# Kernel tuning notes

Measured on AMD Instinct MI355X. Metric: run time of the kernel, lower is better.

## Reference

```python
import jax, jax.numpy as jnp
import numpy as np

B = 2
D = 256
NH = 8
DH = D // NH
LV = 4
NP_ = 4
NL = 6
DFF = 1024
SHAPES = [(112, 112), (56, 56), (28, 28), (14, 14)]
S = sum(h * w for h, w in SHAPES)


def setup_inputs() -> dict:
    key = jax.random.key(0)
    ks = iter(jax.random.split(key, 64))
    d = {}
    for i, (h, w) in enumerate(SHAPES):
        d[f"src{i}"] = jax.random.normal(next(ks), (B, D, h, w), jnp.float32)
        d[f"pos{i}"] = jax.random.normal(next(ks), (B, D, h, w), jnp.float32)

    def W(*shape, scale=0.02):
        return jax.random.normal(next(ks), shape, jnp.float32) * scale

    d["level_embed"] = W(LV, D, scale=1.0)
    d["off_w"] = W(NL, D, NH * LV * NP_ * 2)
    d["off_b"] = W(NL, NH * LV * NP_ * 2, scale=0.5)
    d["aw_w"] = W(NL, D, NH * LV * NP_)
    d["aw_b"] = jnp.zeros((NL, NH * LV * NP_), jnp.float32)
    d["val_w"] = W(NL, D, D)
    d["val_b"] = jnp.zeros((NL, D), jnp.float32)
    d["out_w"] = W(NL, D, D)
    d["out_b"] = jnp.zeros((NL, D), jnp.float32)
    d["ln1_s"] = jnp.ones((NL, D), jnp.float32)
    d["ln1_b"] = jnp.zeros((NL, D), jnp.float32)
    d["ff1_w"] = W(NL, D, DFF)
    d["ff1_b"] = jnp.zeros((NL, DFF), jnp.float32)
    d["ff2_w"] = W(NL, DFF, D)
    d["ff2_b"] = jnp.zeros((NL, D), jnp.float32)
    d["ln2_s"] = jnp.ones((NL, D), jnp.float32)
    d["ln2_b"] = jnp.zeros((NL, D), jnp.float32)
    return d


def _ln(x, s, b):
    m = jnp.mean(x, -1, keepdims=True)
    v = jnp.mean((x - m) ** 2, -1, keepdims=True)
    return (x - m) / jnp.sqrt(v + 1e-5) * s + b


def _bilinear(v, loc, Hl, Wl):
    # v: [N, DH, Hl, Wl]; loc: [N, Q, P, 2] in [0,1] (grid_sample align_corners=False, zero padding)
    N, Dh = v.shape[0], v.shape[1]
    Q, P = loc.shape[1], loc.shape[2]
    x = loc[..., 0] * Wl - 0.5
    y = loc[..., 1] * Hl - 0.5
    x0f = jnp.floor(x)
    y0f = jnp.floor(y)
    lx = x - x0f
    ly = y - y0f
    x0 = x0f.astype(jnp.int32)
    y0 = y0f.astype(jnp.int32)
    vf = v.reshape(N, Dh, Hl * Wl)

    def g(xi, yi):
        valid = (xi >= 0) & (xi < Wl) & (yi >= 0) & (yi < Hl)
        idx = (jnp.clip(yi, 0, Hl - 1) * Wl + jnp.clip(xi, 0, Wl - 1)).reshape(N, Q * P)
        out = jnp.take_along_axis(vf, idx[:, None, :], axis=2).reshape(N, Dh, Q, P)
        return out * valid[:, None].astype(v.dtype)

    w00 = ((1 - lx) * (1 - ly))[:, None]
    w10 = (lx * (1 - ly))[:, None]
    w01 = ((1 - lx) * ly)[:, None]
    w11 = (lx * ly)[:, None]
    return g(x0, y0) * w00 + g(x0 + 1, y0) * w10 + g(x0, y0 + 1) * w01 + g(x0 + 1, y0 + 1) * w11


def _ms_deform_attn(value, loc, attn):
    # value [B,S,NH,DH], loc [B,S,NH,LV,P,2], attn [B,S,NH,LV,P]
    out = jnp.zeros((B * NH, DH, S), value.dtype)
    s0 = 0
    for l, (Hl, Wl) in enumerate(SHAPES):
        vl = value[:, s0:s0 + Hl * Wl].reshape(B, Hl, Wl, NH, DH)
        vl = vl.transpose(0, 3, 4, 1, 2).reshape(B * NH, DH, Hl, Wl)
        ll = loc[:, :, :, l].transpose(0, 2, 1, 3, 4).reshape(B * NH, S, NP_, 2)
        al = attn[:, :, :, l].transpose(0, 2, 1, 3).reshape(B * NH, S, NP_)[:, None]
        out = out + (_bilinear(vl, ll, Hl, Wl) * al).sum(-1)
        s0 += Hl * Wl
    return out.reshape(B, NH * DH, S).transpose(0, 2, 1)


def _forward(srcs, poss, level_embed, off_w, off_b, aw_w, aw_b, val_w, val_b,
             out_w, out_b, ln1_s, ln1_b, ff1_w, ff1_b, ff2_w, ff2_b, ln2_s, ln2_b):
    src = jnp.concatenate([s.reshape(B, D, -1).transpose(0, 2, 1) for s in srcs], 1)
    pos = jnp.concatenate(
        [p.reshape(B, D, -1).transpose(0, 2, 1) + level_embed[i][None, None] for i, p in enumerate(poss)], 1)
    # reference points: padding masks are all-False => valid_ratios == 1
    refs = []
    for (Hl, Wl) in SHAPES:
        gy, gx = jnp.meshgrid((jnp.arange(Hl) + 0.5) / Hl, (jnp.arange(Wl) + 0.5) / Wl, indexing="ij")
        refs.append(jnp.stack([gx.ravel(), gy.ravel()], -1))
    ref = jnp.concatenate(refs, 0)  # [S, 2]
    normalizer = jnp.array([[w, h] for (h, w) in SHAPES], jnp.float32)  # [LV, 2] = (W, H)
    x = src
    for i in range(NL):
        q = x + pos
        off = (q @ off_w[i] + off_b[i]).reshape(B, S, NH, LV, NP_, 2)
        aw = jax.nn.softmax((q @ aw_w[i] + aw_b[i]).reshape(B, S, NH, LV * NP_), -1)
        aw = aw.reshape(B, S, NH, LV, NP_)
        val = (x @ val_w[i] + val_b[i]).reshape(B, S, NH, DH)
        loc = ref[None, :, None, None, None, :] + off / normalizer[None, None, None, :, None, :]
        attn_out = _ms_deform_attn(val, loc, aw) @ out_w[i] + out_b[i]
        x = _ln(x + attn_out, ln1_s[i], ln1_b[i])
        ff = jax.nn.relu(x @ ff1_w[i] + ff1_b[i]) @ ff2_w[i] + ff2_b[i]
        x = _ln(x + ff, ln2_s[i], ln2_b[i])
    return x


def reference(src0, src1, src2, src3, pos0, pos1, pos2, pos3, level_embed,
              off_w, off_b, aw_w, aw_b, val_w, val_b, out_w, out_b,
              ln1_s, ln1_b, ff1_w, ff1_b, ff2_w, ff2_b, ln2_s, ln2_b):
    memory = _forward([src0, src1, src2, src3], [pos0, pos1, pos2, pos3], level_embed,
                      off_w, off_b, aw_w, aw_b, val_w, val_b, out_w, out_b,
                      ln1_s, ln1_b, ff1_w, ff1_b, ff2_w, ff2_b, ln2_s, ln2_b)
    spatial_shapes = jnp.array(SHAPES, jnp.int32)
    level_start_index = jnp.concatenate(
        [jnp.zeros((1,), jnp.int32), jnp.cumsum(spatial_shapes.prod(1))[:-1].astype(jnp.int32)])
    return memory, spatial_shapes, level_start_index
```

## Files before the change

### kernel.cpp

```cpp
#include <hip/hip_runtime.h>


constexpr int kB  = 2;
constexpr int kD  = 256;
constexpr int kNH = 8;
constexpr int kLV = 4;
constexpr int kNP = 4;
constexpr int kNL = 6;
constexpr int kDFF = 1024;
constexpr int kS  = 16660;
constexpr int kM  = kB * kS;
constexpr int kMp = 33408;
constexpr int kMT64 = kMp / 64;
constexpr int kMT32 = kMp / 32;

typedef short bf16x8 __attribute__((ext_vector_type(8)));
typedef float f32x4  __attribute__((ext_vector_type(4)));

__device__ __forceinline__ unsigned short f2bf(float x) {
  union { float f; unsigned int u; } v; v.f = x;
  unsigned int r = v.u + 0x7FFFu + ((v.u >> 16) & 1u);
  return (unsigned short)(r >> 16);
}
__device__ __forceinline__ float bf2f(unsigned short u) {
  union { unsigned int u; float f; } v; v.u = ((unsigned int)u) << 16;
  return v.f;
}
__device__ __forceinline__ float bflo(unsigned int u) {
  union { unsigned int u; float f; } v; v.u = u << 16;
  return v.f;
}
__device__ __forceinline__ float bfhi(unsigned int u) {
  union { unsigned int u; float f; } v; v.u = u & 0xFFFF0000u;
  return v.f;
}

#define GLOAD_LDS16(gp, lp)                                                    \
  __builtin_amdgcn_global_load_lds(                                            \
      (const __attribute__((address_space(1))) void*)(gp),                     \
      (__attribute__((address_space(3))) void*)(lp), 16, 0, 0)

__global__ __launch_bounds__(256) void build_xpos_k(
    const float* __restrict__ src, const float* __restrict__ pos,
    const float* __restrict__ lemb, float* __restrict__ xout,
    float* __restrict__ posout, unsigned short* __restrict__ xbf,
    unsigned short* __restrict__ qbf, int HW, int s0, int lvl)
{
  __shared__ float ts[32][33];
  __shared__ float tp[32][33];
  const int b  = blockIdx.z;
  const int p0 = blockIdx.x * 32, d0 = blockIdx.y * 32;
  const int tx = threadIdx.x, ty = threadIdx.y;
  for (int dd = ty; dd < 32; dd += 8) {
    int p = p0 + tx;
    if (p < HW) {
      size_t idx = ((size_t)b * kD + (d0 + dd)) * (size_t)HW + p;
      ts[dd][tx] = src[idx];
      tp[dd][tx] = pos[idx];
    }
  }
  __syncthreads();
  for (int pp = ty; pp < 32; pp += 8) {
    int p = p0 + pp, d = d0 + tx;
    if (p < HW) {
      size_t o = ((size_t)b * kS + (s0 + p)) * (size_t)kD + d;
      float x = ts[tx][pp];
      float pv = tp[tx][pp] + lemb[lvl * kD + d];
      xout[o] = x;
      posout[o] = pv;
      xbf[o] = f2bf(x);
      qbf[o] = f2bf(x + pv);
    }
  }
}

__global__ __launch_bounds__(256) void wconv_k(
    const float* __restrict__ W, unsigned short* __restrict__ Wt,
    int K, int N, int rowoff, int rowstotal)
{
  __shared__ float t[32][33];
  const int l = blockIdx.z;
  const int n0 = blockIdx.x * 32, k0 = blockIdx.y * 32;
  const int tx = threadIdx.x & 31, ty = threadIdx.x >> 5;
  const float* Wl = W + (size_t)l * K * N;
  unsigned short* Wtl = Wt + (size_t)l * rowstotal * K;
  for (int kk = ty; kk < 32; kk += 8)
    t[kk][tx] = Wl[(size_t)(k0 + kk) * N + n0 + tx];
  __syncthreads();
  for (int nn = ty; nn < 32; nn += 8)
    Wtl[(size_t)(rowoff + n0 + nn) * K + k0 + tx] = f2bf(t[tx][nn]);
}

__global__ __launch_bounds__(256) void biaspack_k(
    const float* __restrict__ ob, const float* __restrict__ ab,
    float* __restrict__ qb)
{
  int i = blockIdx.x * 256 + threadIdx.x;
  if (i >= kNL * 384) return;
  int l = i / 384, c = i - l * 384;
  qb[i] = (c < 256) ? ob[l * 256 + c] : ab[l * 128 + (c - 256)];
}

template<int RELU, int OUTBF>
__global__ __launch_bounds__(256) void hgemm64_k(
    const unsigned short* __restrict__ A, const unsigned short* __restrict__ Bt,
    const float* __restrict__ bias, void* __restrict__ Cout, int N, int K)
{
  __shared__ unsigned short As[2][64 * 32];
  __shared__ unsigned short Bs[2][128 * 32];
  const int tid = threadIdx.x;
  const int bm = blockIdx.y * 64;
  const int bn = blockIdx.x * 128;
  const int lane = tid & 63;
  const int wave = tid >> 6;
  const int wr = (wave >> 1) * 32, wc = (wave & 1) * 64;
  const int l15 = lane & 15, l4 = lane >> 4;

  f32x4 acc[2][4] = {};

  const unsigned short* A0 = A + (size_t)(bm + (tid >> 2)) * K + ((tid & 3) << 3);
  const int cb1 = 256 + tid;
  const unsigned short* B0 = Bt + (size_t)(bn + (tid >> 2)) * K + ((tid & 3) << 3);
  const unsigned short* B1 = Bt + (size_t)(bn + (cb1 >> 2)) * K + ((cb1 & 3) << 3);

#define STAGE64(buf, k0)                                                       \
  do {                                                                         \
    GLOAD_LDS16(A0 + (k0), (char*)As[buf] + tid * 16);                         \
    GLOAD_LDS16(B0 + (k0), (char*)Bs[buf] + tid * 16);                         \
    GLOAD_LDS16(B1 + (k0), (char*)Bs[buf] + cb1 * 16);                         \
  } while (0)

  STAGE64(0, 0);
  __syncthreads();
  int cur = 0;
  for (int k0 = 0; k0 < K; k0 += 32) {
    if (k0 + 32 < K) STAGE64(cur ^ 1, k0 + 32);
    bf16x8 af[2], bfr[4];
#pragma unroll
    for (int m = 0; m < 2; ++m)
      af[m] = *(const bf16x8*)&As[cur][(wr + m * 16 + l15) * 32 + l4 * 8];
#pragma unroll
    for (int n = 0; n < 4; ++n)
      bfr[n] = *(const bf16x8*)&Bs[cur][(wc + n * 16 + l15) * 32 + l4 * 8];
#pragma unroll
    for (int m = 0; m < 2; ++m)
#pragma unroll
      for (int n = 0; n < 4; ++n)
        acc[m][n] = __builtin_amdgcn_mfma_f32_16x16x32_bf16(
            af[m], bfr[n], acc[m][n], 0, 0, 0);
    __syncthreads();
    cur ^= 1;
  }
#undef STAGE64

#pragma unroll
  for (int n = 0; n < 4; ++n) {
    const int col = bn + wc + n * 16 + l15;
    const float bv = bias[col];
#pragma unroll
    for (int m = 0; m < 2; ++m) {
#pragma unroll
      for (int j = 0; j < 4; ++j) {
        const int row = bm + wr + m * 16 + l4 * 4 + j;
        float v = acc[m][n][j] + bv;
        if (RELU) v = fmaxf(v, 0.f);
        if (OUTBF)
          ((unsigned short*)Cout)[(size_t)row * N + col] = f2bf(v);
        else
          ((float*)Cout)[(size_t)row * N + col] = v;
      }
    }
  }
}

__global__ __launch_bounds__(256) void qvgemm_k(
    const unsigned short* __restrict__ Aq, const unsigned short* __restrict__ Ax,
    const unsigned short* __restrict__ Bq, const unsigned short* __restrict__ Bv,
    const float* __restrict__ biasq, const float* __restrict__ biasv,
    float* __restrict__ Cq, unsigned short* __restrict__ Cv)
{
  constexpr int K = 256;
  __shared__ unsigned short As[2][64 * 32];
  __shared__ unsigned short Bs[2][128 * 32];
  const int tid = threadIdx.x;
  const int bx = blockIdx.x;
  const bool isv = bx >= 3;
  const int bn = (isv ? bx - 3 : bx) * 128;
  const int bm = blockIdx.y * 64;
  const unsigned short* A  = isv ? Ax : Aq;
  const unsigned short* Bt = isv ? Bv : Bq;
  const float* bias = isv ? biasv : biasq;
  const int N = isv ? 256 : 384;
  const int lane = tid & 63;
  const int wave = tid >> 6;
  const int wr = (wave >> 1) * 32, wc = (wave & 1) * 64;
  const int l15 = lane & 15, l4 = lane >> 4;

  f32x4 acc[2][4] = {};

  const unsigned short* A0 = A + (size_t)(bm + (tid >> 2)) * K + ((tid & 3) << 3);
  const int cb1 = 256 + tid;
  const unsigned short* B0 = Bt + (size_t)(bn + (tid >> 2)) * K + ((tid & 3) << 3);
  const unsigned short* B1 = Bt + (size_t)(bn + (cb1 >> 2)) * K + ((cb1 & 3) << 3);

#define STAGEQV(buf, k0)                                                       \
  do {                                                                         \
    GLOAD_LDS16(A0 + (k0), (char*)As[buf] + tid * 16);                         \
    GLOAD_LDS16(B0 + (k0), (char*)Bs[buf] + tid * 16);                         \
    GLOAD_LDS16(B1 + (k0), (char*)Bs[buf] + cb1 * 16);                         \
  } while (0)

  STAGEQV(0, 0);
  __syncthreads();
  int cur = 0;
#pragma unroll
  for (int k0 = 0; k0 < K; k0 += 32) {
    if (k0 + 32 < K) STAGEQV(cur ^ 1, k0 + 32);
    bf16x8 af[2], bfr[4];
#pragma unroll
    for (int m = 0; m < 2; ++m)
      af[m] = *(const bf16x8*)&As[cur][(wr + m * 16 + l15) * 32 + l4 * 8];
#pragma unroll
    for (int n = 0; n < 4; ++n)
      bfr[n] = *(const bf16x8*)&Bs[cur][(wc + n * 16 + l15) * 32 + l4 * 8];
#pragma unroll
    for (int m = 0; m < 2; ++m)
#pragma unroll
      for (int n = 0; n < 4; ++n)
        acc[m][n] = __builtin_amdgcn_mfma_f32_16x16x32_bf16(
            af[m], bfr[n], acc[m][n], 0, 0, 0);
    __syncthreads();
    cur ^= 1;
  }
#undef STAGEQV

#pragma unroll
  for (int n = 0; n < 4; ++n) {
    const int col = bn + wc + n * 16 + l15;
    const float bv = bias[col];
#pragma unroll
    for (int m = 0; m < 2; ++m) {
#pragma unroll
      for (int j = 0; j < 4; ++j) {
        const int row = bm + wr + m * 16 + l4 * 4 + j;
        float v = acc[m][n][j] + bv;
        if (isv)
          Cv[(size_t)row * 256 + col] = f2bf(v);
        else
          Cq[(size_t)row * 384 + col] = v;
      }
    }
  }
}

template<int WQ, int OUTDST>
__global__ __launch_bounds__(256) void hgemmln_k(
    const unsigned short* __restrict__ A, const unsigned short* __restrict__ Bt,
    const float* __restrict__ bias, const float* __restrict__ Rsd,
    const float* __restrict__ g, const float* __restrict__ beta,
    const float* __restrict__ posb, float* __restrict__ yout,
    unsigned short* __restrict__ xbf, unsigned short* __restrict__ qbf, int K)
{
  __shared__ unsigned short As[2][32 * 32];
  __shared__ unsigned short Bs[2][256 * 32];
  __shared__ float ssum[32][5];
  __shared__ float ssq[32][5];
  const int tid = threadIdx.x;
  const int bm = blockIdx.x * 32;
  const int lane = tid & 63;
  const int wave = tid >> 6;
  const int wc = wave * 64;
  const int l15 = lane & 15, l4 = lane >> 4;

  f32x4 acc[2][4] = {};

  const unsigned short* Aq = A + (size_t)(bm + (tid >> 2)) * K + ((tid & 3) << 3);
  const unsigned short* Bq0 = Bt + (size_t)(0 * 64 + (tid >> 2)) * K + ((tid & 3) << 3);
  const unsigned short* Bq1 = Bt + (size_t)(1 * 64 + (tid >> 2)) * K + ((tid & 3) << 3);
  const unsigned short* Bq2 = Bt + (size_t)(2 * 64 + (tid >> 2)) * K + ((tid & 3) << 3);
  const unsigned short* Bq3 = Bt + (size_t)(3 * 64 + (tid >> 2)) * K + ((tid & 3) << 3);

#define STAGE_LN(buf, k0)                                                      \
  do {                                                                         \
    if (tid < 128) GLOAD_LDS16(Aq + (k0), (char*)As[buf] + tid * 16);          \
    GLOAD_LDS16(Bq0 + (k0), (char*)Bs[buf] + (0 * 256 + tid) * 16);            \
    GLOAD_LDS16(Bq1 + (k0), (char*)Bs[buf] + (1 * 256 + tid) * 16);            \
    GLOAD_LDS16(Bq2 + (k0), (char*)Bs[buf] + (2 * 256 + tid) * 16);            \
    GLOAD_LDS16(Bq3 + (k0), (char*)Bs[buf] + (3 * 256 + tid) * 16);            \
  } while (0)

  STAGE_LN(0, 0);
  __syncthreads();
  int cur = 0;
  for (int k0 = 0; k0 < K; k0 += 32) {
    if (k0 + 32 < K) STAGE_LN(cur ^ 1, k0 + 32);
    bf16x8 af[2], bfr[4];
#pragma unroll
    for (int m = 0; m < 2; ++m)
      af[m] = *(const bf16x8*)&As[cur][(m * 16 + l15) * 32 + l4 * 8];
#pragma unroll
    for (int n = 0; n < 4; ++n)
      bfr[n] = *(const bf16x8*)&Bs[cur][(wc + n * 16 + l15) * 32 + l4 * 8];
#pragma unroll
    for (int m = 0; m < 2; ++m)
#pragma unroll
      for (int n = 0; n < 4; ++n)
        acc[m][n] = __builtin_amdgcn_mfma_f32_16x16x32_bf16(
            af[m], bfr[n], acc[m][n], 0, 0, 0);
    __syncthreads();
    cur ^= 1;
  }
#undef STAGE_LN

  float bv[4], gv[4], btv[4];
#pragma unroll
  for (int n = 0; n < 4; ++n) {
    const int col = wc + n * 16 + l15;
    bv[n] = bias[col];
    gv[n] = g[col];
    btv[n] = beta[col];
  }
#pragma unroll
  for (int m = 0; m < 2; ++m) {
#pragma unroll
    for (int j = 0; j < 4; ++j) {
      const int row = bm + m * 16 + l4 * 4 + j;
#pragma unroll
      for (int n = 0; n < 4; ++n)
        acc[m][n][j] += bv[n] + Rsd[(size_t)row * kD + wc + n * 16 + l15];
    }
  }
#pragma unroll
  for (int m = 0; m < 2; ++m) {
#pragma unroll
    for (int j = 0; j < 4; ++j) {
      float s = acc[m][0][j] + acc[m][1][j] + acc[m][2][j] + acc[m][3][j];
      float q = acc[m][0][j] * acc[m][0][j] + acc[m][1][j] * acc[m][1][j] +
                acc[m][2][j] * acc[m][2][j] + acc[m][3][j] * acc[m][3][j];
#pragma unroll
      for (int d2 = 1; d2 < 16; d2 <<= 1) {
        s += __shfl_xor(s, d2, 64);
        q += __shfl_xor(q, d2, 64);
      }
      if (l15 == 0) {
        const int r = m * 16 + l4 * 4 + j;
        ssum[r][wave] = s;
        ssq[r][wave] = q;
      }
    }
  }
  __syncthreads();
#pragma unroll
  for (int m = 0; m < 2; ++m) {
#pragma unroll
    for (int j = 0; j < 4; ++j) {
      const int r = m * 16 + l4 * 4 + j;
      const int row = bm + r;
      const float mean = (ssum[r][0] + ssum[r][1] + ssum[r][2] + ssum[r][3]) *
                         (1.0f / kD);
      const float var = (ssq[r][0] + ssq[r][1] + ssq[r][2] + ssq[r][3]) *
                        (1.0f / kD) - mean * mean;
      const float rstd = rsqrtf(var + 1e-5f);
      if (row < kM) {
#pragma unroll
        for (int n = 0; n < 4; ++n) {
          const int col = wc + n * 16 + l15;
          const float y = (acc[m][n][j] - mean) * rstd * gv[n] + btv[n];
          const size_t o = (size_t)row * kD + col;
          if (OUTDST) {
            yout[o] = y;
          } else {
            yout[o] = y;
            xbf[o] = f2bf(y);
            if (WQ) qbf[o] = f2bf(y + posb[o]);
          }
        }
      }
    }
  }
}

__global__ __launch_bounds__(256) void msdeform_k(
    const unsigned short* __restrict__ val, const float* __restrict__ qout,
    unsigned short* __restrict__ outbf)
{
  __shared__ int   sIdx[4][4][128];
  __shared__ float sW[4][4][128];
  const int bs0 = blockIdx.x * 4;
  const int tid = threadIdx.x;

#pragma unroll
  for (int it = 0; it < 2; ++it) {
    const int item = tid + it * 256;
    const int q = item >> 7;
    const int t = item & 127;
    const int bs = bs0 + q;
    const int b = bs / kS, s = bs - b * kS;
    const int l = (t & 15) >> 2;

    const float logit = qout[(size_t)bs * 384 + 256 + t];
    float mx = logit;
#pragma unroll
    for (int d2 = 1; d2 < 16; d2 <<= 1) mx = fmaxf(mx, __shfl_xor(mx, d2, 64));
    float e = __expf(logit - mx);
    float sm = e;
#pragma unroll
    for (int d2 = 1; d2 < 16; d2 <<= 1) sm += __shfl_xor(sm, d2, 64);
    const float a = e / sm;

    int ls, sideq;
    if (s < 12544)      { ls = s;         sideq = 112; }
    else if (s < 15680) { ls = s - 12544; sideq = 56;  }
    else if (s < 16464) { ls = s - 15680; sideq = 28;  }
    else                { ls = s - 16464; sideq = 14;  }
    const float rx = ((ls % sideq) + 0.5f) / (float)sideq;
    const float ry = ((ls / sideq) + 0.5f) / (float)sideq;

    const int side  = 112 >> l;
    const int start = (l >= 1 ? 12544 : 0) + (l >= 2 ? 3136 : 0) + (l >= 3 ? 784 : 0);
    const float ox = qout[(size_t)bs * 384 + t * 2 + 0];
    const float oy = qout[(size_t)bs * 384 + t * 2 + 1];
    const float xx = rx * side + ox - 0.5f;
    const float yy = ry * side + oy - 0.5f;
    const float xf = floorf(xx), yf = floorf(yy);
    const float lx = xx - xf, ly = yy - yf;
    const int x0 = (int)xf, y0 = (int)yf;
    const float w00 = (1.f - lx) * (1.f - ly) * a, w10 = lx * (1.f - ly) * a;
    const float w01 = (1.f - lx) * ly * a,         w11 = lx * ly * a;
    const bool xv0 = (unsigned)x0 < (unsigned)side, xv1 = (unsigned)(x0 + 1) < (unsigned)side;
    const bool yv0 = (unsigned)y0 < (unsigned)side, yv1 = (unsigned)(y0 + 1) < (unsigned)side;
    const int cx0 = min(max(x0, 0), side - 1), cx1 = min(max(x0 + 1, 0), side - 1);
    const int cy0 = min(max(y0, 0), side - 1), cy1 = min(max(y0 + 1, 0), side - 1);
    const int rowbase = b * kS + start;
    const int t2 = (t & 15) * 8 + (t >> 4);
    sIdx[0][q][t2] = (rowbase + cy0 * side + cx0) * 512;
    sIdx[1][q][t2] = (rowbase + cy0 * side + cx1) * 512;
    sIdx[2][q][t2] = (rowbase + cy1 * side + cx0) * 512;
    sIdx[3][q][t2] = (rowbase + cy1 * side + cx1) * 512;
    sW[0][q][t2] = (xv0 && yv0) ? w00 : 0.f;
    sW[1][q][t2] = (xv1 && yv0) ? w10 : 0.f;
    sW[2][q][t2] = (xv0 && yv1) ? w01 : 0.f;
    sW[3][q][t2] = (xv1 && yv1) ? w11 : 0.f;
  }
  __syncthreads();

  const int q    = tid >> 6;
  const int lane = tid & 63;
  const int h    = lane >> 3;
  const int l4   = (lane >> 1) & 3;
  const int cp   = lane & 1;
  const char* vbase = (const char*)val + h * 64 + l4 * 16;

  float a0 = 0.f, a1 = 0.f, a2 = 0.f, a3 = 0.f;
  float a4 = 0.f, a5 = 0.f, a6 = 0.f, a7 = 0.f;
#pragma unroll
  for (int sp = 0; sp < 16; ++sp) {
    const int t2 = sp * 8 + h;
#pragma unroll
    for (int j = 0; j < 2; ++j) {
      const int c = 2 * cp + j;
      const int off = sIdx[c][q][t2];
      const float w = sW[c][q][t2];
      const uint4 v = *(const uint4*)(vbase + off);
      a0 = fmaf(w, bflo(v.x), a0); a1 = fmaf(w, bfhi(v.x), a1);
      a2 = fmaf(w, bflo(v.y), a2); a3 = fmaf(w, bfhi(v.y), a3);
      a4 = fmaf(w, bflo(v.z), a4); a5 = fmaf(w, bfhi(v.z), a5);
      a6 = fmaf(w, bflo(v.w), a6); a7 = fmaf(w, bfhi(v.w), a7);
    }
  }
  a0 += __shfl_xor(a0, 1, 64); a1 += __shfl_xor(a1, 1, 64);
  a2 += __shfl_xor(a2, 1, 64); a3 += __shfl_xor(a3, 1, 64);
  a4 += __shfl_xor(a4, 1, 64); a5 += __shfl_xor(a5, 1, 64);
  a6 += __shfl_xor(a6, 1, 64); a7 += __shfl_xor(a7, 1, 64);
  if (cp == 0) {
    bf16x8 o;
    o[0] = (short)f2bf(a0); o[1] = (short)f2bf(a1);
    o[2] = (short)f2bf(a2); o[3] = (short)f2bf(a3);
    o[4] = (short)f2bf(a4); o[5] = (short)f2bf(a5);
    o[6] = (short)f2bf(a6); o[7] = (short)f2bf(a7);
    *(bf16x8*)(outbf + (size_t)(bs0 + q) * 256 + h * 32 + l4 * 8) = o;
  }
}

__global__ void tail_k(float* __restrict__ out)
{
  if (threadIdx.x == 0) {
    const size_t n = (size_t)kM * kD;
    out[n + 0] = 112.f; out[n + 1] = 112.f;
    out[n + 2] = 56.f;  out[n + 3] = 56.f;
    out[n + 4] = 28.f;  out[n + 5] = 28.f;
    out[n + 6] = 14.f;  out[n + 7] = 14.f;
    out[n + 8] = 0.f;   out[n + 9] = 12544.f;
    out[n + 10] = 15680.f; out[n + 11] = 16464.f;
  }
}

extern "C" void kernel_launch(void* const* d_in, const int* in_sizes, int n_in,
                              void* d_out, int out_size, void* d_ws, size_t ws_size,
                              hipStream_t stream)
{
  const float* src[4] = {(const float*)d_in[0], (const float*)d_in[2],
                         (const float*)d_in[4], (const float*)d_in[6]};
  const float* pos[4] = {(const float*)d_in[1], (const float*)d_in[3],
                         (const float*)d_in[5], (const float*)d_in[7]};
  const float* lemb  = (const float*)d_in[8];
  const float* off_w = (const float*)d_in[9];
  const float* off_b = (const float*)d_in[10];
  const float* aw_w  = (const float*)d_in[11];
  const float* aw_b  = (const float*)d_in[12];
  const float* val_w = (const float*)d_in[13];
  const float* val_b = (const float*)d_in[14];
  const float* out_w = (const float*)d_in[15];
  const float* out_b = (const float*)d_in[16];
  const float* ln1_s = (const float*)d_in[17];
  const float* ln1_b = (const float*)d_in[18];
  const float* ff1_w = (const float*)d_in[19];
  const float* ff1_b = (const float*)d_in[20];
  const float* ff2_w = (const float*)d_in[21];
  const float* ff2_b = (const float*)d_in[22];
  const float* ln2_s = (const float*)d_in[23];
  const float* ln2_b = (const float*)d_in[24];

  const size_t SZ = (size_t)kMp * kD;
  float* ws   = (float*)d_ws;
  float* posb = (float*)d_out;
  float* xb   = ws;
  float* R    = ws + SZ;
  float* qout = R;
  unsigned short* valbf = (unsigned short*)(R + SZ + SZ / 2);
  unsigned short* attbf = (unsigned short*)(R + 2 * SZ);
  unsigned short* ffbf  = (unsigned short*)R;
  unsigned short* qbf   = (unsigned short*)(ws + 3 * SZ + SZ / 2);
  unsigned short* xbf   = qbf + SZ;
  unsigned short* wts   = (unsigned short*)(ws + 4 * SZ + SZ / 2);
  unsigned short* qwT  = wts;
  unsigned short* valT = qwT + kNL * 384 * 256;
  unsigned short* outT = valT + kNL * 256 * 256;
  unsigned short* ff1T = outT + kNL * 256 * 256;
  unsigned short* ff2T = ff1T + kNL * 1024 * 256;
  float* qbias = (float*)(ff2T + kNL * 256 * 1024);

  wconv_k<<<dim3(256 / 32, 256 / 32, kNL), 256, 0, stream>>>(off_w, qwT, 256, 256, 0, 384);
  wconv_k<<<dim3(128 / 32, 256 / 32, kNL), 256, 0, stream>>>(aw_w,  qwT, 256, 128, 256, 384);
  wconv_k<<<dim3(256 / 32, 256 / 32, kNL), 256, 0, stream>>>(val_w, valT, 256, 256, 0, 256);
  wconv_k<<<dim3(256 / 32, 256 / 32, kNL), 256, 0, stream>>>(out_w, outT, 256, 256, 0, 256);
  wconv_k<<<dim3(1024 / 32, 256 / 32, kNL), 256, 0, stream>>>(ff1_w, ff1T, 256, 1024, 0, 1024);
  wconv_k<<<dim3(256 / 32, 1024 / 32, kNL), 256, 0, stream>>>(ff2_w, ff2T, 1024, 256, 0, 256);
  biaspack_k<<<(kNL * 384 + 255) / 256, 256, 0, stream>>>(off_b, aw_b, qbias);

  const int sides[4]  = {112, 56, 28, 14};
  const int starts[4] = {0, 12544, 15680, 16464};
  for (int l = 0; l < 4; ++l) {
    int HW = sides[l] * sides[l];
    dim3 g((HW + 31) / 32, kD / 32, kB);
    build_xpos_k<<<g, dim3(32, 8), 0, stream>>>(src[l], pos[l], lemb, xb, posb,
                                                xbf, qbf, HW, starts[l], l);
  }

  const dim3 blk(256);
  for (int i = 0; i < kNL; ++i) {
    qvgemm_k<<<dim3(5, kMT64), blk, 0, stream>>>(
        qbf, xbf, qwT + (size_t)i * 384 * 256, valT + (size_t)i * 256 * 256,
        qbias + i * 384, val_b + i * 256, qout, valbf);
    msdeform_k<<<kM / 4, blk, 0, stream>>>(valbf, qout, attbf);
    hgemmln_k<0, 0><<<kMT32, blk, 0, stream>>>(
        attbf, outT + (size_t)i * 256 * 256, out_b + i * 256, xb,
        ln1_s + i * kD, ln1_b + i * kD, nullptr, xb, xbf, nullptr, 256);
    hgemm64_k<1, 1><<<dim3(8, kMT64), blk, 0, stream>>>(
        xbf, ff1T + (size_t)i * 1024 * 256, ff1_b + i * 1024, ffbf, 1024, 256);
    if (i < kNL - 1) {
      hgemmln_k<1, 0><<<kMT32, blk, 0, stream>>>(
          ffbf, ff2T + (size_t)i * 256 * 1024, ff2_b + i * 256, xb,
          ln2_s + i * kD, ln2_b + i * kD, posb, xb, xbf, qbf, 1024);
    } else {
      hgemmln_k<0, 1><<<kMT32, blk, 0, stream>>>(
          ffbf, ff2T + (size_t)i * 256 * 1024, ff2_b + i * 256, xb,
          ln2_s + i * kD, ln2_b + i * kD, nullptr, (float*)d_out, nullptr,
          nullptr, 1024);
    }
  }

  tail_k<<<1, 64, 0, stream>>>((float*)d_out);
}
```

Before: 1.566 ms.

## Store value projection in fp32 and precompute reference point table

The value projection output is now written as fp32 instead of bf16. The deformable-attention gather reads float4 per lane across all four bilinear corners, which removes the two-lane split and the shuffle reduction. Reference coordinates are precomputed once into a table, replacing per-thread level and division arithmetic. The cost is double the value-tensor bytes for both the write and the scattered gathers, plus a workspace layout shift.

```diff
diff --git a/kernel.cpp b/kernel.cpp
--- a/kernel.cpp
+++ b/kernel.cpp
@@ -26,14 +26,6 @@
   union { unsigned int u; float f; } v; v.u = ((unsigned int)u) << 16;
   return v.f;
 }
-__device__ __forceinline__ float bflo(unsigned int u) {
-  union { unsigned int u; float f; } v; v.u = u << 16;
-  return v.f;
-}
-__device__ __forceinline__ float bfhi(unsigned int u) {
-  union { unsigned int u; float f; } v; v.u = u & 0xFFFF0000u;
-  return v.f;
-}
 
 #define GLOAD_LDS16(gp, lp)                                                    \
   __builtin_amdgcn_global_load_lds(                                            \
@@ -101,6 +93,20 @@
   qb[i] = (c < 256) ? ob[l * 256 + c] : ab[l * 128 + (c - 256)];
 }
 
+__global__ __launch_bounds__(256) void refxy_k(float* __restrict__ ref)
+{
+  int s = blockIdx.x * 256 + threadIdx.x;
+  if (s >= kS) return;
+  int ls, side;
+  if (s < 12544)      { ls = s;         side = 112; }
+  else if (s < 15680) { ls = s - 12544; side = 56;  }
+  else if (s < 16464) { ls = s - 15680; side = 28;  }
+  else                { ls = s - 16464; side = 14;  }
+  const float inv = 1.0f / (float)side;
+  ref[s * 2 + 0] = ((ls % side) + 0.5f) * inv;
+  ref[s * 2 + 1] = ((ls / side) + 0.5f) * inv;
+}
+
 template<int RELU, int OUTBF>
 __global__ __launch_bounds__(256) void hgemm64_k(
     const unsigned short* __restrict__ A, const unsigned short* __restrict__ Bt,
@@ -177,7 +183,7 @@
     const unsigned short* __restrict__ Aq, const unsigned short* __restrict__ Ax,
     const unsigned short* __restrict__ Bq, const unsigned short* __restrict__ Bv,
     const float* __restrict__ biasq, const float* __restrict__ biasv,
-    float* __restrict__ Cq, unsigned short* __restrict__ Cv)
+    float* __restrict__ Cq, float* __restrict__ Cv)
 {
   constexpr int K = 256;
   __shared__ unsigned short As[2][64 * 32];
@@ -190,7 +196,6 @@
   const unsigned short* A  = isv ? Ax : Aq;
   const unsigned short* Bt = isv ? Bv : Bq;
   const float* bias = isv ? biasv : biasq;
-  const int N = isv ? 256 : 384;
   const int lane = tid & 63;
   const int wave = tid >> 6;
   const int wr = (wave >> 1) * 32, wc = (wave & 1) * 64;
@@ -245,7 +250,7 @@
         const int row = bm + wr + m * 16 + l4 * 4 + j;
         float v = acc[m][n][j] + bv;
         if (isv)
-          Cv[(size_t)row * 256 + col] = f2bf(v);
+          Cv[(size_t)row * 256 + col] = v;
         else
           Cq[(size_t)row * 384 + col] = v;
       }
@@ -381,8 +386,8 @@
 }
 
 __global__ __launch_bounds__(256) void msdeform_k(
-    const unsigned short* __restrict__ val, const float* __restrict__ qout,
-    unsigned short* __restrict__ outbf)
+    const float* __restrict__ valf, const float* __restrict__ qout,
+    const float* __restrict__ ref, unsigned short* __restrict__ outbf)
 {
   __shared__ int   sIdx[4][4][128];
   __shared__ float sW[4][4][128];
@@ -408,20 +413,14 @@
     for (int d2 = 1; d2 < 16; d2 <<= 1) sm += __shfl_xor(sm, d2, 64);
     const float a = e / sm;
 
-    int ls, sideq;
-    if (s < 12544)      { ls = s;         sideq = 112; }
-    else if (s < 15680) { ls = s - 12544; sideq = 56;  }
-    else if (s < 16464) { ls = s - 15680; sideq = 28;  }
-    else                { ls = s - 16464; sideq = 14;  }
-    const float rx = ((ls % sideq) + 0.5f) / (float)sideq;
-    const float ry = ((ls / sideq) + 0.5f) / (float)sideq;
-
+    const float rfx = ref[s * 2 + 0];
+    const float rfy = ref[s * 2 + 1];
     const int side  = 112 >> l;
     const int start = (l >= 1 ? 12544 : 0) + (l >= 2 ? 3136 : 0) + (l >= 3 ? 784 : 0);
     const float ox = qout[(size_t)bs * 384 + t * 2 + 0];
     const float oy = qout[(size_t)bs * 384 + t * 2 + 1];
-    const float xx = rx * side + ox - 0.5f;
-    const float yy = ry * side + oy - 0.5f;
+    const float xx = fmaf(rfx, (float)side, ox) - 0.5f;
+    const float yy = fmaf(rfy, (float)side, oy) - 0.5f;
     const float xf = floorf(xx), yf = floorf(yy);
     const float lx = xx - xf, ly = yy - yf;
     const int x0 = (int)xf, y0 = (int)yf;
@@ -433,10 +432,10 @@
     const int cy0 = min(max(y0, 0), side - 1), cy1 = min(max(y0 + 1, 0), side - 1);
     const int rowbase = b * kS + start;
     const int t2 = (t & 15) * 8 + (t >> 4);
-    sIdx[0][q][t2] = (rowbase + cy0 * side + cx0) * 512;
-    sIdx[1][q][t2] = (rowbase + cy0 * side + cx1) * 512;
-    sIdx[2][q][t2] = (rowbase + cy1 * side + cx0) * 512;
-    sIdx[3][q][t2] = (rowbase + cy1 * side + cx1) * 512;
+    sIdx[0][q][t2] = (rowbase + cy0 * side + cx0) << 10;
+    sIdx[1][q][t2] = (rowbase + cy0 * side + cx1) << 10;
+    sIdx[2][q][t2] = (rowbase + cy1 * side + cx0) << 10;
+    sIdx[3][q][t2] = (rowbase + cy1 * side + cx1) << 10;
     sW[0][q][t2] = (xv0 && yv0) ? w00 : 0.f;
     sW[1][q][t2] = (xv1 && yv0) ? w10 : 0.f;
     sW[2][q][t2] = (xv0 && yv1) ? w01 : 0.f;
@@ -444,42 +443,29 @@
   }
   __syncthreads();
 
-  const int q    = tid >> 6;
-  const int lane = tid & 63;
-  const int h    = lane >> 3;
-  const int l4   = (lane >> 1) & 3;
-  const int cp   = lane & 1;
-  const char* vbase = (const char*)val + h * 64 + l4 * 16;
+  const int q  = tid >> 6;
+  const int h  = (tid >> 3) & 7;
+  const int l8 = tid & 7;
+  const char* vbase = (const char*)valf + h * 128 + l8 * 16;
 
   float a0 = 0.f, a1 = 0.f, a2 = 0.f, a3 = 0.f;
-  float a4 = 0.f, a5 = 0.f, a6 = 0.f, a7 = 0.f;
 #pragma unroll
   for (int sp = 0; sp < 16; ++sp) {
     const int t2 = sp * 8 + h;
 #pragma unroll
-    for (int j = 0; j < 2; ++j) {
-      const int c = 2 * cp + j;
+    for (int c = 0; c < 4; ++c) {
       const int off = sIdx[c][q][t2];
       const float w = sW[c][q][t2];
-      const uint4 v = *(const uint4*)(vbase + off);
-      a0 = fmaf(w, bflo(v.x), a0); a1 = fmaf(w, bfhi(v.x), a1);
-      a2 = fmaf(w, bflo(v.y), a2); a3 = fmaf(w, bfhi(v.y), a3);
-      a4 = fmaf(w, bflo(v.z), a4); a5 = fmaf(w, bfhi(v.z), a5);
-      a6 = fmaf(w, bflo(v.w), a6); a7 = fmaf(w, bfhi(v.w), a7);
-    }
-  }
-  a0 += __shfl_xor(a0, 1, 64); a1 += __shfl_xor(a1, 1, 64);
-  a2 += __shfl_xor(a2, 1, 64); a3 += __shfl_xor(a3, 1, 64);
-  a4 += __shfl_xor(a4, 1, 64); a5 += __shfl_xor(a5, 1, 64);
-  a6 += __shfl_xor(a6, 1, 64); a7 += __shfl_xor(a7, 1, 64);
-  if (cp == 0) {
-    bf16x8 o;
-    o[0] = (short)f2bf(a0); o[1] = (short)f2bf(a1);
-    o[2] = (short)f2bf(a2); o[3] = (short)f2bf(a3);
-    o[4] = (short)f2bf(a4); o[5] = (short)f2bf(a5);
-    o[6] = (short)f2bf(a6); o[7] = (short)f2bf(a7);
-    *(bf16x8*)(outbf + (size_t)(bs0 + q) * 256 + h * 32 + l4 * 8) = o;
-  }
+      const float4 v = *(const float4*)(vbase + off);
+      a0 = fmaf(w, v.x, a0);
+      a1 = fmaf(w, v.y, a1);
+      a2 = fmaf(w, v.z, a2);
+      a3 = fmaf(w, v.w, a3);
+    }
+  }
+  ushort4 o;
+  o.x = f2bf(a0); o.y = f2bf(a1); o.z = f2bf(a2); o.w = f2bf(a3);
+  *(ushort4*)(outbf + (size_t)(bs0 + q) * 256 + h * 32 + l8 * 4) = o;
 }
 
 __global__ void tail_k(float* __restrict__ out)
@@ -527,18 +513,19 @@
   float* xb   = ws;
   float* R    = ws + SZ;
   float* qout = R;
-  unsigned short* valbf = (unsigned short*)(R + SZ + SZ / 2);
-  unsigned short* attbf = (unsigned short*)(R + 2 * SZ);
+  float* valf = R + SZ + SZ / 2;
+  unsigned short* attbf = (unsigned short*)(R + 2 * SZ + SZ / 2);
   unsigned short* ffbf  = (unsigned short*)R;
-  unsigned short* qbf   = (unsigned short*)(ws + 3 * SZ + SZ / 2);
+  unsigned short* qbf   = (unsigned short*)(ws + 4 * SZ);
   unsigned short* xbf   = qbf + SZ;
-  unsigned short* wts   = (unsigned short*)(ws + 4 * SZ + SZ / 2);
+  unsigned short* wts   = (unsigned short*)(ws + 5 * SZ);
   unsigned short* qwT  = wts;
   unsigned short* valT = qwT + kNL * 384 * 256;
   unsigned short* outT = valT + kNL * 256 * 256;
   unsigned short* ff1T = outT + kNL * 256 * 256;
   unsigned short* ff2T = ff1T + kNL * 1024 * 256;
   float* qbias = (float*)(ff2T + kNL * 256 * 1024);
+  float* reftab = qbias + kNL * 384;
 
   wconv_k<<<dim3(256 / 32, 256 / 32, kNL), 256, 0, stream>>>(off_w, qwT, 256, 256, 0, 384);
   wconv_k<<<dim3(128 / 32, 256 / 32, kNL), 256, 0, stream>>>(aw_w,  qwT, 256, 128, 256, 384);
@@ -547,6 +534,7 @@
   wconv_k<<<dim3(1024 / 32, 256 / 32, kNL), 256, 0, stream>>>(ff1_w, ff1T, 256, 1024, 0, 1024);
   wconv_k<<<dim3(256 / 32, 1024 / 32, kNL), 256, 0, stream>>>(ff2_w, ff2T, 1024, 256, 0, 256);
   biaspack_k<<<(kNL * 384 + 255) / 256, 256, 0, stream>>>(off_b, aw_b, qbias);
+  refxy_k<<<(kS + 255) / 256, 256, 0, stream>>>(reftab);
 
   const int sides[4]  = {112, 56, 28, 14};
   const int starts[4] = {0, 12544, 15680, 16464};
@@ -561,8 +549,8 @@
   for (int i = 0; i < kNL; ++i) {
     qvgemm_k<<<dim3(5, kMT64), blk, 0, stream>>>(
         qbf, xbf, qwT + (size_t)i * 384 * 256, valT + (size_t)i * 256 * 256,
-        qbias + i * 384, val_b + i * 256, qout, valbf);
-    msdeform_k<<<kM / 4, blk, 0, stream>>>(valbf, qout, attbf);
+        qbias + i * 384, val_b + i * 256, qout, valf);
+    msdeform_k<<<kM / 4, blk, 0, stream>>>(valf, qout, reftab, attbf);
     hgemmln_k<0, 0><<<kMT32, blk, 0, stream>>>(
         attbf, outT + (size_t)i * 256 * 256, out_b + i * 256, xb,
         ln1_s + i * kD, ln1_b + i * kD, nullptr, xb, xbf, nullptr, 256);
```

After: 1.587 ms. Within noise of the previous version (+1.4%).

## Process eight queries per msdeform block and precompute reference points

Applied to the files above, without the earlier changes.

The deformable-attention kernel now handles 8 queries per block instead of 4. Each thread owns one 8-channel slice and accumulates all four bilinear corners itself, so the cross-lane shuffle reduction and the half-idle store are gone. Reference coordinates are computed once by a new kernel into a table rather than being recomputed with integer divides in every layer. The workspace is also compacted. The cost is larger shared-memory arrays, fewer blocks, and more serial loads per thread.

```diff
diff --git a/kernel.cpp b/kernel.cpp
--- a/kernel.cpp
+++ b/kernel.cpp
@@ -101,6 +101,20 @@
   qb[i] = (c < 256) ? ob[l * 256 + c] : ab[l * 128 + (c - 256)];
 }
 
+__global__ __launch_bounds__(256) void refxy_k(float* __restrict__ ref)
+{
+  int s = blockIdx.x * 256 + threadIdx.x;
+  if (s >= kS) return;
+  int ls, side;
+  if (s < 12544)      { ls = s;         side = 112; }
+  else if (s < 15680) { ls = s - 12544; side = 56;  }
+  else if (s < 16464) { ls = s - 15680; side = 28;  }
+  else                { ls = s - 16464; side = 14;  }
+  const float inv = 1.0f / (float)side;
+  ref[s * 2 + 0] = ((ls % side) + 0.5f) * inv;
+  ref[s * 2 + 1] = ((ls / side) + 0.5f) * inv;
+}
+
 template<int RELU, int OUTBF>
 __global__ __launch_bounds__(256) void hgemm64_k(
     const unsigned short* __restrict__ A, const unsigned short* __restrict__ Bt,
@@ -190,7 +204,6 @@
   const unsigned short* A  = isv ? Ax : Aq;
   const unsigned short* Bt = isv ? Bv : Bq;
   const float* bias = isv ? biasv : biasq;
-  const int N = isv ? 256 : 384;
   const int lane = tid & 63;
   const int wave = tid >> 6;
   const int wr = (wave >> 1) * 32, wc = (wave & 1) * 64;
@@ -382,15 +395,15 @@
 
 __global__ __launch_bounds__(256) void msdeform_k(
     const unsigned short* __restrict__ val, const float* __restrict__ qout,
-    unsigned short* __restrict__ outbf)
-{
-  __shared__ int   sIdx[4][4][128];
-  __shared__ float sW[4][4][128];
-  const int bs0 = blockIdx.x * 4;
+    const float* __restrict__ ref, unsigned short* __restrict__ outbf)
+{
+  __shared__ int   sIdx[4][8][128];
+  __shared__ float sW[4][8][128];
+  const int bs0 = blockIdx.x * 8;
   const int tid = threadIdx.x;
 
 #pragma unroll
-  for (int it = 0; it < 2; ++it) {
+  for (int it = 0; it < 4; ++it) {
     const int item = tid + it * 256;
     const int q = item >> 7;
     const int t = item & 127;
@@ -408,20 +421,14 @@
     for (int d2 = 1; d2 < 16; d2 <<= 1) sm += __shfl_xor(sm, d2, 64);
     const float a = e / sm;
 
-    int ls, sideq;
-    if (s < 12544)      { ls = s;         sideq = 112; }
-    else if (s < 15680) { ls = s - 12544; sideq = 56;  }
-    else if (s < 16464) { ls = s - 15680; sideq = 28;  }
-    else                { ls = s - 16464; sideq = 14;  }
-    const float rx = ((ls % sideq) + 0.5f) / (float)sideq;
-    const float ry = ((ls / sideq) + 0.5f) / (float)sideq;
-
+    const float rfx = ref[s * 2 + 0];
+    const float rfy = ref[s * 2 + 1];
     const int side  = 112 >> l;
     const int start = (l >= 1 ? 12544 : 0) + (l >= 2 ? 3136 : 0) + (l >= 3 ? 784 : 0);
     const float ox = qout[(size_t)bs * 384 + t * 2 + 0];
     const float oy = qout[(size_t)bs * 384 + t * 2 + 1];
-    const float xx = rx * side + ox - 0.5f;
-    const float yy = ry * side + oy - 0.5f;
+    const float xx = fmaf(rfx, (float)side, ox) - 0.5f;
+    const float yy = fmaf(rfy, (float)side, oy) - 0.5f;
     const float xf = floorf(xx), yf = floorf(yy);
     const float lx = xx - xf, ly = yy - yf;
     const int x0 = (int)xf, y0 = (int)yf;
@@ -433,10 +440,10 @@
     const int cy0 = min(max(y0, 0), side - 1), cy1 = min(max(y0 + 1, 0), side - 1);
     const int rowbase = b * kS + start;
     const int t2 = (t & 15) * 8 + (t >> 4);
-    sIdx[0][q][t2] = (rowbase + cy0 * side + cx0) * 512;
-    sIdx[1][q][t2] = (rowbase + cy0 * side + cx1) * 512;
-    sIdx[2][q][t2] = (rowbase + cy1 * side + cx0) * 512;
-    sIdx[3][q][t2] = (rowbase + cy1 * side + cx1) * 512;
+    sIdx[0][q][t2] = (rowbase + cy0 * side + cx0) << 9;
+    sIdx[1][q][t2] = (rowbase + cy0 * side + cx1) << 9;
+    sIdx[2][q][t2] = (rowbase + cy1 * side + cx0) << 9;
+    sIdx[3][q][t2] = (rowbase + cy1 * side + cx1) << 9;
     sW[0][q][t2] = (xv0 && yv0) ? w00 : 0.f;
     sW[1][q][t2] = (xv1 && yv0) ? w10 : 0.f;
     sW[2][q][t2] = (xv0 && yv1) ? w01 : 0.f;
@@ -444,11 +451,9 @@
   }
   __syncthreads();
 
-  const int q    = tid >> 6;
-  const int lane = tid & 63;
-  const int h    = lane >> 3;
-  const int l4   = (lane >> 1) & 3;
-  const int cp   = lane & 1;
+  const int q  = tid >> 5;
+  const int h  = (tid >> 2) & 7;
+  const int l4 = tid & 3;
   const char* vbase = (const char*)val + h * 64 + l4 * 16;
 
   float a0 = 0.f, a1 = 0.f, a2 = 0.f, a3 = 0.f;
@@ -457,8 +462,7 @@
   for (int sp = 0; sp < 16; ++sp) {
     const int t2 = sp * 8 + h;
 #pragma unroll
-    for (int j = 0; j < 2; ++j) {
-      const int c = 2 * cp + j;
+    for (int c = 0; c < 4; ++c) {
       const int off = sIdx[c][q][t2];
       const float w = sW[c][q][t2];
       const uint4 v = *(const uint4*)(vbase + off);
@@ -468,18 +472,12 @@
       a6 = fmaf(w, bflo(v.w), a6); a7 = fmaf(w, bfhi(v.w), a7);
     }
   }
-  a0 += __shfl_xor(a0, 1, 64); a1 += __shfl_xor(a1, 1, 64);
-  a2 += __shfl_xor(a2, 1, 64); a3 += __shfl_xor(a3, 1, 64);
-  a4 += __shfl_xor(a4, 1, 64); a5 += __shfl_xor(a5, 1, 64);
-  a6 += __shfl_xor(a6, 1, 64); a7 += __shfl_xor(a7, 1, 64);
-  if (cp == 0) {
-    bf16x8 o;
-    o[0] = (short)f2bf(a0); o[1] = (short)f2bf(a1);
-    o[2] = (short)f2bf(a2); o[3] = (short)f2bf(a3);
-    o[4] = (short)f2bf(a4); o[5] = (short)f2bf(a5);
-    o[6] = (short)f2bf(a6); o[7] = (short)f2bf(a7);
-    *(bf16x8*)(outbf + (size_t)(bs0 + q) * 256 + h * 32 + l4 * 8) = o;
-  }
+  bf16x8 o;
+  o[0] = (short)f2bf(a0); o[1] = (short)f2bf(a1);
+  o[2] = (short)f2bf(a2); o[3] = (short)f2bf(a3);
+  o[4] = (short)f2bf(a4); o[5] = (short)f2bf(a5);
+  o[6] = (short)f2bf(a6); o[7] = (short)f2bf(a7);
+  *(bf16x8*)(outbf + (size_t)(bs0 + q) * 256 + h * 32 + l4 * 8) = o;
 }
 
 __global__ void tail_k(float* __restrict__ out)
@@ -530,15 +528,16 @@
   unsigned short* valbf = (unsigned short*)(R + SZ + SZ / 2);
   unsigned short* attbf = (unsigned short*)(R + 2 * SZ);
   unsigned short* ffbf  = (unsigned short*)R;
-  unsigned short* qbf   = (unsigned short*)(ws + 3 * SZ + SZ / 2);
+  unsigned short* qbf   = (unsigned short*)(ws + 3 * SZ);
   unsigned short* xbf   = qbf + SZ;
-  unsigned short* wts   = (unsigned short*)(ws + 4 * SZ + SZ / 2);
+  unsigned short* wts   = (unsigned short*)(ws + 4 * SZ);
   unsigned short* qwT  = wts;
   unsigned short* valT = qwT + kNL * 384 * 256;
   unsigned short* outT = valT + kNL * 256 * 256;
   unsigned short* ff1T = outT + kNL * 256 * 256;
   unsigned short* ff2T = ff1T + kNL * 1024 * 256;
   float* qbias = (float*)(ff2T + kNL * 256 * 1024);
+  float* reftab = qbias + kNL * 384;
 
   wconv_k<<<dim3(256 / 32, 256 / 32, kNL), 256, 0, stream>>>(off_w, qwT, 256, 256, 0, 384);
   wconv_k<<<dim3(128 / 32, 256 / 32, kNL), 256, 0, stream>>>(aw_w,  qwT, 256, 128, 256, 384);
@@ -547,6 +546,7 @@
   wconv_k<<<dim3(1024 / 32, 256 / 32, kNL), 256, 0, stream>>>(ff1_w, ff1T, 256, 1024, 0, 1024);
   wconv_k<<<dim3(256 / 32, 1024 / 32, kNL), 256, 0, stream>>>(ff2_w, ff2T, 1024, 256, 0, 256);
   biaspack_k<<<(kNL * 384 + 255) / 256, 256, 0, stream>>>(off_b, aw_b, qbias);
+  refxy_k<<<(kS + 255) / 256, 256, 0, stream>>>(reftab);
 
   const int sides[4]  = {112, 56, 28, 14};
   const int starts[4] = {0, 12544, 15680, 16464};
@@ -562,7 +562,7 @@
     qvgemm_k<<<dim3(5, kMT64), blk, 0, stream>>>(
         qbf, xbf, qwT + (size_t)i * 384 * 256, valT + (size_t)i * 256 * 256,
         qbias + i * 384, val_b + i * 256, qout, valbf);
-    msdeform_k<<<kM / 4, blk, 0, stream>>>(valbf, qout, attbf);
+    msdeform_k<<<kM / 8, blk, 0, stream>>>(valbf, qout, reftab, attbf);
     hgemmln_k<0, 0><<<kMT32, blk, 0, stream>>>(
         attbf, outT + (size_t)i * 256 * 256, out_b + i * 256, xb,
         ln1_s + i * kD, ln1_b + i * kD, nullptr, xb, xbf, nullptr, 256);
```

After: 1.443 ms. 7.8% less time.
